# Optimization experiments

Hardware: AMD Instinct MI355X
Metric: run time of the kernel (lower is better)

Reference implementation:

```python
import jax, jax.numpy as jnp
import numpy as np

B, NQ, NK = 4, 2048, 2048
D_MODEL, H, DK, DV, M = 512, 8, 64, 64, 40


def setup_inputs() -> dict:
    key = jax.random.key(0)
    ks = jax.random.split(key, 12)
    s = 0.02  # param init scale (stand-in for xavier)
    return {
        "queries": jax.random.normal(ks[0], (B, NQ, D_MODEL), jnp.float32),
        "keys": jax.random.normal(ks[1], (B, NK, D_MODEL), jnp.float32),
        "values": jax.random.normal(ks[2], (B, NK, D_MODEL), jnp.float32),
        "attention_weights": jax.random.uniform(ks[3], (B, H, NQ, NK), jnp.float32),
        "attention_mask": jax.random.randint(ks[4], (B, H, NQ, NK), 0, 2) == 1,
        "Wq": jax.random.normal(ks[5], (D_MODEL, H * DK), jnp.float32) * s,
        "bq": jnp.zeros((H * DK,), jnp.float32),
        "Wk": jax.random.normal(ks[6], (D_MODEL, H * DK), jnp.float32) * s,
        "bk": jnp.zeros((H * DK,), jnp.float32),
        "Wv": jax.random.normal(ks[7], (D_MODEL, H * DV), jnp.float32) * s,
        "bv": jnp.zeros((H * DV,), jnp.float32),
        "Wo": jax.random.normal(ks[8], (H * DV, D_MODEL), jnp.float32) * s,
        "bo": jnp.zeros((D_MODEL,), jnp.float32),
        "m_k": jax.random.normal(ks[9], (1, M, H * DK), jnp.float32) * s,
        "m_v": jax.random.normal(ks[10], (1, M, H * DV), jnp.float32) * s,
    }


def reference(queries, keys, values, attention_weights, attention_mask,
              Wq, bq, Wk, bk, Wv, bv, Wo, bo, m_k, m_v):
    b, nq, _ = queries.shape
    nk = keys.shape[1]
    # learned memory slots, scaled and broadcast over batch
    mk = jnp.sqrt(jnp.float32(DK)) * jnp.broadcast_to(m_k, (b, M, H * DK))
    mv = jnp.sqrt(jnp.float32(M)) * jnp.broadcast_to(m_v, (b, M, H * DV))
    q = (queries @ Wq + bq).reshape(b, nq, H, DK).transpose(0, 2, 1, 3)      # (b,h,nq,dk)
    k = jnp.concatenate([keys @ Wk + bk, mk], axis=1)
    k = k.reshape(b, nk + M, H, DK).transpose(0, 2, 3, 1)                     # (b,h,dk,nk+m)
    v = jnp.concatenate([values @ Wv + bv, mv], axis=1)
    v = v.reshape(b, nk + M, H, DV).transpose(0, 2, 1, 3)                     # (b,h,nk+m,dv)
    att = jnp.matmul(q, k) / jnp.sqrt(jnp.float32(DK))                        # (b,h,nq,nk+m)
    att_x = att[..., :nk] * attention_weights
    att_x = jnp.where(attention_mask, -jnp.inf, att_x)
    att = jnp.concatenate([att_x, att[..., nk:]], axis=-1)
    att = jax.nn.softmax(att, axis=-1)
    out = jnp.matmul(att, v).transpose(0, 2, 1, 3).reshape(b, nq, H * DV)
    return out @ Wo + bo
```

## Files before the change

kernel.cpp:

```cpp
#include <hip/hip_runtime.h>
#include <hip/hip_bf16.h>
#include <cstdint>
#include <cstddef>

typedef __bf16 bf16_t;
typedef __bf16 bf16x8 __attribute__((ext_vector_type(8)));
typedef __bf16 bf16x4 __attribute__((ext_vector_type(4)));
typedef float  f32x4  __attribute__((ext_vector_type(4)));

#define B_    4
#define NQ_   2048
#define NK_   2048
#define H_    8
#define MSL_  40
#define NKP_  2112
#define SCL2  0.18033688011112042f

#define GLOAD_LDS16(GP, LP)                                                        \
    __builtin_amdgcn_global_load_lds(                                              \
        (const __attribute__((address_space(1))) unsigned int*)(GP),               \
        (__attribute__((address_space(3))) unsigned int*)(LP), 16, 0, 0)

__global__ void detect_mask(const unsigned int* __restrict__ m, int* __restrict__ flag)
{
    __shared__ int found;
    if (threadIdx.x == 0) found = 0;
    __syncthreads();
    unsigned int acc = 0;
    for (int i = threadIdx.x; i < 65536; i += 256)
        acc |= (m[i] & 0xFFFFFF00u);
    if (acc) found = 1;
    __syncthreads();
    if (threadIdx.x == 0) *flag = found;
}

__global__ void transpose_convert4(const float* __restrict__ s0, const float* __restrict__ s1,
                                   const float* __restrict__ s2, const float* __restrict__ s3,
                                   bf16_t* __restrict__ d0, bf16_t* __restrict__ d1,
                                   bf16_t* __restrict__ d2, bf16_t* __restrict__ d3)
{
    const float* src; bf16_t* dst;
    switch (blockIdx.z) {
        case 0:  src = s0; dst = d0; break;
        case 1:  src = s1; dst = d1; break;
        case 2:  src = s2; dst = d2; break;
        default: src = s3; dst = d3; break;
    }
    __shared__ float t[32][33];
    int x  = blockIdx.x * 32 + threadIdx.x;
    int y0 = blockIdx.y * 32 + threadIdx.y;
#pragma unroll
    for (int i = 0; i < 32; i += 8)
        t[threadIdx.y + i][threadIdx.x] = src[(size_t)(y0 + i) * 512 + x];
    __syncthreads();
    int ox  = blockIdx.y * 32 + threadIdx.x;
    int oy0 = blockIdx.x * 32 + threadIdx.y;
#pragma unroll
    for (int i = 0; i < 32; i += 8)
        dst[(size_t)(oy0 + i) * 512 + ox] = (bf16_t)t[threadIdx.x][threadIdx.y + i];
}

__global__ void memfill(const float* __restrict__ m_k, const float* __restrict__ m_v,
                        bf16_t* __restrict__ Kbf, bf16_t* __restrict__ Vt)
{
    int tid = blockIdx.x * 256 + threadIdx.x;
    if (tid < 4 * 64 * 512) {
        int c  = tid & 511;
        int mi = (tid >> 9) & 63;
        int b  = tid >> 15;
        float v = (mi < MSL_) ? 8.0f * m_k[mi * 512 + c] : 0.0f;
        Kbf[((size_t)b * NKP_ + NK_ + mi) * 512 + c] = (bf16_t)v;
    } else {
        int t  = tid - 4 * 64 * 512;
        int mi = t & 63;
        int dv = (t >> 6) & 63;
        int h  = (t >> 12) & 7;
        int b  = t >> 15;
        float v = (mi < MSL_) ? 6.324555320336759f * m_v[mi * 512 + h * 64 + dv] : 0.0f;
        Vt[(((size_t)b * H_ + h) * 64 + dv) * NKP_ + NK_ + mi] = (bf16_t)v;
    }
}

template<int EPI, bool AF32>
__global__ __launch_bounds__(256) void gemm_bt(
    const void* __restrict__ Av, const bf16_t* __restrict__ BT,
    const float* __restrict__ bias, void* __restrict__ dstv, int dstBS)
{
    __shared__ bf16_t As[128][72];
    __shared__ bf16_t Bs[128][72];

    const int tid = threadIdx.x;
    const int w = tid >> 6, l = tid & 63, lg = l >> 4, lr = l & 15;
    const int wr = w >> 1, wc = w & 1;
    const int blockM = blockIdx.x * 128, blockN = blockIdx.y * 128;

    f32x4 acc[4][4];
    const f32x4 zv = {0.f, 0.f, 0.f, 0.f};
#pragma unroll
    for (int i = 0; i < 4; i++)
#pragma unroll
        for (int j = 0; j < 4; j++) acc[i][j] = zv;

    const int ar = tid >> 1;
    const int ac = (tid & 1) * 32;

    for (int k0 = 0; k0 < 512; k0 += 64) {
        if (k0) __syncthreads();
        if constexpr (AF32) {
            const float* arow = (const float*)Av + (size_t)(blockM + ar) * 512 + k0 + ac;
#pragma unroll
            for (int i = 0; i < 8; i++) {
                float4 v = ((const float4*)arow)[i];
                bf16x4 pk = {(bf16_t)v.x, (bf16_t)v.y, (bf16_t)v.z, (bf16_t)v.w};
                *(bf16x4*)&As[ar][ac + i * 4] = pk;
            }
        } else {
            const bf16_t* arow = (const bf16_t*)Av + (size_t)(blockM + ar) * 512 + k0 + ac;
#pragma unroll
            for (int i = 0; i < 4; i++)
                *(uint4*)&As[ar][ac + i * 8] = ((const uint4*)arow)[i];
        }
        {
            const bf16_t* brow = BT + (size_t)(blockN + ar) * 512 + k0 + ac;
#pragma unroll
            for (int i = 0; i < 4; i++)
                *(uint4*)&Bs[ar][ac + i * 8] = ((const uint4*)brow)[i];
        }
        __syncthreads();
#pragma unroll
        for (int ks = 0; ks < 2; ks++) {
            bf16x8 af[4], bfr[4];
#pragma unroll
            for (int mi = 0; mi < 4; mi++)
                af[mi] = *(const bf16x8*)&As[wr * 64 + mi * 16 + lr][ks * 32 + lg * 8];
#pragma unroll
            for (int ni = 0; ni < 4; ni++)
                bfr[ni] = *(const bf16x8*)&Bs[wc * 64 + ni * 16 + lr][ks * 32 + lg * 8];
#pragma unroll
            for (int mi = 0; mi < 4; mi++)
#pragma unroll
                for (int ni = 0; ni < 4; ni++)
                    acc[mi][ni] = __builtin_amdgcn_mfma_f32_16x16x32_bf16(af[mi], bfr[ni], acc[mi][ni], 0, 0, 0);
        }
    }

    const int colbase = blockN + wc * 64;
    float bias_v[4];
#pragma unroll
    for (int ni = 0; ni < 4; ni++) bias_v[ni] = bias[colbase + ni * 16 + lr];

#pragma unroll
    for (int mi = 0; mi < 4; mi++) {
        const int r0 = blockM + wr * 64 + mi * 16 + lg * 4;
#pragma unroll
        for (int ni = 0; ni < 4; ni++) {
            const int c = colbase + ni * 16 + lr;
            f32x4 v = acc[mi][ni];
            if constexpr (EPI == 2) {
                float* dst = (float*)dstv;
#pragma unroll
                for (int j = 0; j < 4; j++)
                    dst[(size_t)(r0 + j) * 512 + c] = v[j] + bias_v[ni];
            } else if constexpr (EPI == 0) {
                bf16_t* dst = (bf16_t*)dstv;
#pragma unroll
                for (int j = 0; j < 4; j++) {
                    int rr = r0 + j;
                    int bb = rr >> 11, nn = rr & 2047;
                    dst[((size_t)bb * dstBS + nn) * 512 + c] = (bf16_t)(v[j] + bias_v[ni]);
                }
            } else {
                bf16_t* dst = (bf16_t*)dstv;
                int bb = r0 >> 11, n0 = r0 & 2047;
                int hh = c >> 6, dv = c & 63;
                bf16x4 pk;
#pragma unroll
                for (int j = 0; j < 4; j++) pk[j] = (bf16_t)(v[j] + bias_v[ni]);
                *(bf16x4*)(dst + (((size_t)bb * H_ + hh) * 64 + dv) * NKP_ + n0) = pk;
            }
        }
    }
}

template<bool BYTEM>
__global__ __launch_bounds__(256) void attn_fused(
    const bf16_t* __restrict__ Qbf, const bf16_t* __restrict__ Kbf,
    const bf16_t* __restrict__ Vt, const float* __restrict__ attw,
    const void* __restrict__ maskv, const int* __restrict__ mflag,
    bf16_t* __restrict__ Obuf)
{
    if ((*mflag != 0) != BYTEM) return;

    __shared__ bf16_t Ks[2][64][64];
    __shared__ bf16_t Vs[2][64][64];
    __shared__ bf16_t Pl[4][1024];

    const int tid = threadIdx.x;
    const int wv = tid >> 6, l = tid & 63, lg = l >> 4, lr = l & 15;
    const int qt = blockIdx.x, h = blockIdx.y, b = blockIdx.z;
    const int q0w = qt * 64 + wv * 16;
    bf16_t* Pw = &Pl[wv][0];

    const size_t bh = (size_t)(b * H_ + h);
    const float* wbase = attw + bh * (size_t)NQ_ * NK_;
    const unsigned char* mb8 = (const unsigned char*)maskv + bh * (size_t)NQ_ * NK_;
    const int* mb32 = (const int*)maskv + bh * (size_t)NQ_ * NK_;
    const char* kbase8 = (const char*)(Kbf + (size_t)b * NKP_ * 512 + h * 64);
    const char* vbase8 = (const char*)(Vt + bh * 64 * (size_t)NKP_);

    bf16x8 qf0 = *(const bf16x8*)&Qbf[((size_t)b * NQ_ + q0w + lr) * 512 + h * 64 + lg * 8];
    bf16x8 qf1 = *(const bf16x8*)&Qbf[((size_t)b * NQ_ + q0w + lr) * 512 + h * 64 + 32 + lg * 8];

    const f32x4 zv = {0.f, 0.f, 0.f, 0.f};
    f32x4 oacc[4];
#pragma unroll
    for (int i = 0; i < 4; i++) oacc[i] = zv;
    float mrun = -INFINITY, lsum = 0.f;
    f32x4 sA[4];

    f32x4 wA[4], wB[4];
    unsigned mA[4], mB[4];
    unsigned miA[16], miB[16];

    const int srow = l >> 3;
    const int scsw = ((l & 7) ^ (srow & 7)) * 16;

#define STAGE(BUF, KCB) do {                                                      \
    _Pragma("unroll") for (int pi_ = 0; pi_ < 2; pi_++) {                         \
        const int p_ = wv * 2 + pi_;                                              \
        const int r_ = p_ * 8 + srow;                                             \
        GLOAD_LDS16(kbase8 + (size_t)((KCB) + r_) * 1024 + scsw,                  \
                    (char*)&Ks[BUF][0][0] + p_ * 1024);                           \
        GLOAD_LDS16(vbase8 + (size_t)r_ * 4224 + (size_t)(KCB) * 2 + scsw,        \
                    (char*)&Vs[BUF][0][0] + p_ * 1024);                           \
    }                                                                             \
} while (0)

#define PREFETCH(KT, WB_, MB_, MIB_) do {                                         \
    const float* wp_ = wbase + (size_t)(q0w + lr) * NK_ + (KT) * 64 + lg * 4;     \
    _Pragma("unroll") for (int n_ = 0; n_ < 4; n_++)                              \
        WB_[n_] = *(const f32x4*)(wp_ + n_ * 16);                                 \
    if constexpr (BYTEM) {                                                        \
        const unsigned char* mp_ = mb8 + (size_t)(q0w + lr) * NK_ + (KT) * 64 + lg * 4; \
        _Pragma("unroll") for (int n_ = 0; n_ < 4; n_++)                          \
            MB_[n_] = *(const unsigned*)(mp_ + n_ * 16);                          \
    } else {                                                                      \
        const int* mp_ = mb32 + (size_t)(q0w + lr) * NK_ + (KT) * 64 + lg * 4;    \
        _Pragma("unroll") for (int n_ = 0; n_ < 4; n_++) {                        \
            uint4 t_ = *(const uint4*)(mp_ + n_ * 16);                            \
            MIB_[n_ * 4 + 0] = t_.x; MIB_[n_ * 4 + 1] = t_.y;                     \
            MIB_[n_ * 4 + 2] = t_.z; MIB_[n_ * 4 + 3] = t_.w; }                   \
    }                                                                             \
} while (0)

#define QKT_LDS(BC) do {                                                          \
    const int sw_ = (lg ^ (lr & 7)) * 8;                                          \
    _Pragma("unroll") for (int n_ = 0; n_ < 4; n_++) {                            \
        const int kr_ = n_ * 16 + lr;                                             \
        f32x4 a_ = zv;                                                            \
        a_ = __builtin_amdgcn_mfma_f32_16x16x32_bf16(*(const bf16x8*)&Ks[BC][kr_][sw_], qf0, a_, 0, 0, 0); \
        a_ = __builtin_amdgcn_mfma_f32_16x16x32_bf16(*(const bf16x8*)&Ks[BC][kr_][sw_ ^ 32], qf1, a_, 0, 0, 0); \
        sA[n_] = a_;                                                              \
    }                                                                             \
} while (0)

#define APPLY(WB_, MB_, MIB_) do {                                                \
    _Pragma("unroll") for (int n_ = 0; n_ < 4; n_++)                              \
    _Pragma("unroll") for (int j_ = 0; j_ < 4; j_++) {                            \
        bool mk_;                                                                 \
        if constexpr (BYTEM) mk_ = ((MB_[n_] >> (8 * j_)) & 0xffu) != 0;          \
        else                 mk_ = (MIB_[n_ * 4 + j_] != 0);                      \
        sA[n_][j_] = mk_ ? -1e30f : sA[n_][j_] * SCL2 * WB_[n_][j_];              \
    }                                                                             \
} while (0)

#define SMPV(BC) do {                                                             \
    float tm_ = sA[0][0];                                                         \
    _Pragma("unroll") for (int n_ = 0; n_ < 4; n_++)                              \
    _Pragma("unroll") for (int j_ = 0; j_ < 4; j_++)                              \
        tm_ = fmaxf(tm_, sA[n_][j_]);                                             \
    tm_ = fmaxf(tm_, __shfl_xor(tm_, 16));                                        \
    tm_ = fmaxf(tm_, __shfl_xor(tm_, 32));                                        \
    float mnew_ = fmaxf(mrun, tm_);                                               \
    float sc_ = exp2f(mrun - mnew_);                                              \
    mrun = mnew_;                                                                 \
    float ts_ = 0.f;                                                              \
    _Pragma("unroll") for (int n_ = 0; n_ < 4; n_++)                              \
    _Pragma("unroll") for (int j_ = 0; j_ < 4; j_++) {                            \
        float p_ = exp2f(sA[n_][j_] - mnew_);                                     \
        sA[n_][j_] = p_; ts_ += p_;                                               \
    }                                                                             \
    ts_ += __shfl_xor(ts_, 16);                                                   \
    ts_ += __shfl_xor(ts_, 32);                                                   \
    lsum = lsum * sc_ + ts_;                                                      \
    _Pragma("unroll") for (int n2_ = 0; n2_ < 4; n2_++) oacc[n2_] *= sc_;         \
    _Pragma("unroll") for (int n_ = 0; n_ < 4; n_++) {                            \
        int c_ = n_ * 2 + (lg >> 1);                                              \
        int qp_ = (lr + 4 * c_) & 15;                                             \
        bf16x4 pk_ = {(bf16_t)sA[n_][0], (bf16_t)sA[n_][1],                       \
                      (bf16_t)sA[n_][2], (bf16_t)sA[n_][3]};                      \
        *(bf16x4*)&Pw[c_ * 128 + qp_ * 8 + (lg & 1) * 4] = pk_;                   \
    }                                                                             \
    bf16x8 pf0_ = *(const bf16x8*)&Pw[lg * 128 + ((lr + 4 * lg) & 15) * 8];       \
    bf16x8 pf1_ = *(const bf16x8*)&Pw[(4 + lg) * 128 + ((lr + 4 * (4 + lg)) & 15) * 8]; \
    const int vsw_ = (lg ^ (lr & 7)) * 8;                                         \
    _Pragma("unroll") for (int n2_ = 0; n2_ < 4; n2_++) {                         \
        const int vr_ = n2_ * 16 + lr;                                            \
        oacc[n2_] = __builtin_amdgcn_mfma_f32_16x16x32_bf16(*(const bf16x8*)&Vs[BC][vr_][vsw_], pf0_, oacc[n2_], 0, 0, 0); \
        oacc[n2_] = __builtin_amdgcn_mfma_f32_16x16x32_bf16(*(const bf16x8*)&Vs[BC][vr_][vsw_ ^ 32], pf1_, oacc[n2_], 0, 0, 0); \
    }                                                                             \
} while (0)

#define BODYT(KT, BC, BN, WB_, MB_, MIB_, WN_, MN_, MIN_) do {                    \
    if ((KT) < 31) STAGE(BN, ((KT) + 1) * 64);                                    \
    QKT_LDS(BC);                                                                  \
    if ((KT) < 31) PREFETCH((KT) + 1, WN_, MN_, MIN_);                            \
    APPLY(WB_, MB_, MIB_);                                                        \
    SMPV(BC);                                                                     \
    __syncthreads();                                                              \
} while (0)

    STAGE(0, 2048);
    PREFETCH(0, wA, mA, miA);
    __syncthreads();

    {
        STAGE(1, 0);
        QKT_LDS(0);
#pragma unroll
        for (int n_ = 0; n_ < 4; n_++)
#pragma unroll
            for (int j_ = 0; j_ < 4; j_++) {
                int kloc = n_ * 16 + lg * 4 + j_;
                sA[n_][j_] = (kloc >= MSL_) ? -1e30f : sA[n_][j_] * SCL2;
            }
        SMPV(0);
        __syncthreads();
    }

    for (int kt = 0; kt < 32; kt += 2) {
        BODYT(kt,     1, 0, wA, mA, miA, wB, mB, miB);
        BODYT(kt + 1, 0, 1, wB, mB, miB, wA, mA, miA);
    }

    float invl = 1.0f / lsum;
#pragma unroll
    for (int n2 = 0; n2 < 4; n2++) {
        bf16x4 ov = {(bf16_t)(oacc[n2][0] * invl), (bf16_t)(oacc[n2][1] * invl),
                     (bf16_t)(oacc[n2][2] * invl), (bf16_t)(oacc[n2][3] * invl)};
        *(bf16x4*)&Obuf[((size_t)b * NQ_ + q0w + lr) * 512 + h * 64 + n2 * 16 + lg * 4] = ov;
    }

#undef STAGE
#undef PREFETCH
#undef QKT_LDS
#undef APPLY
#undef SMPV
#undef BODYT
}

extern "C" void kernel_launch(void* const* d_in, const int* in_sizes, int n_in,
                              void* d_out, int out_size, void* d_ws, size_t ws_size,
                              hipStream_t stream)
{
    const float* queries = (const float*)d_in[0];
    const float* keys    = (const float*)d_in[1];
    const float* values  = (const float*)d_in[2];
    const float* attw    = (const float*)d_in[3];
    const void*  maskv   = d_in[4];
    const float* Wq = (const float*)d_in[5];
    const float* bq = (const float*)d_in[6];
    const float* Wk = (const float*)d_in[7];
    const float* bk = (const float*)d_in[8];
    const float* Wv = (const float*)d_in[9];
    const float* bv = (const float*)d_in[10];
    const float* Wo = (const float*)d_in[11];
    const float* bo = (const float*)d_in[12];
    const float* m_k = (const float*)d_in[13];
    const float* m_v = (const float*)d_in[14];

    char* ws = (char*)d_ws;
    bf16_t* WqT  = (bf16_t*)(ws + 0);
    bf16_t* WkT  = (bf16_t*)(ws + 524288);
    bf16_t* WvT  = (bf16_t*)(ws + 1048576);
    bf16_t* WoT  = (bf16_t*)(ws + 1572864);
    bf16_t* Qbf  = (bf16_t*)(ws + 2097152);
    bf16_t* Kbf  = (bf16_t*)(ws + 10485760);
    bf16_t* Vt   = (bf16_t*)(ws + 19136512);
    bf16_t* Obuf = (bf16_t*)(ws + 27787264);
    int*    mflag = (int*)(ws + 36175872);

    detect_mask<<<1, 256, 0, stream>>>((const unsigned int*)maskv, mflag);
    transpose_convert4<<<dim3(16, 16, 4), dim3(32, 8), 0, stream>>>(
        Wq, Wk, Wv, Wo, WqT, WkT, WvT, WoT);
    memfill<<<1024, 256, 0, stream>>>(m_k, m_v, Kbf, Vt);

    gemm_bt<0, true><<<dim3(64, 4), 256, 0, stream>>>(queries, WqT, bq, Qbf, 2048);
    gemm_bt<0, true><<<dim3(64, 4), 256, 0, stream>>>(keys,    WkT, bk, Kbf, NKP_);
    gemm_bt<1, true><<<dim3(64, 4), 256, 0, stream>>>(values,  WvT, bv, Vt, 0);

    attn_fused<true><<<dim3(32, H_, B_), 256, 0, stream>>>(Qbf, Kbf, Vt, attw, maskv, mflag, Obuf);
    attn_fused<false><<<dim3(32, H_, B_), 256, 0, stream>>>(Qbf, Kbf, Vt, attw, maskv, mflag, Obuf);

    gemm_bt<2, false><<<dim3(64, 4), 256, 0, stream>>>(Obuf, WoT, bo, d_out, 0);
    (void)in_sizes; (void)n_in; (void)out_size; (void)ws_size;
}
```

Baseline: 381.4 us.

## Deepen attention pipeline with two-tile-ahead prefetch and partial vmcnt waits

Restructures the attention main loop so the attention-weight/mask register prefetch runs two tiles ahead instead of one. The end-of-iteration __syncthreads is replaced by a start-of-iteration s_waitcnt vmcnt(8) plus s_barrier, so outstanding global loads are not fully drained. sched_barriers pin the instruction order so the compiler cannot move loads across the staging points. The aim is to hide global memory latency for K/V staging and the attw/mask streams. The hand-tuned vmcnt count is fragile: it depends on exactly how many loads each stage issues, and a wrong count could race on LDS.

```diff
diff --git a/kernel.cpp b/kernel.cpp
--- a/kernel.cpp
+++ b/kernel.cpp
@@ -311,21 +311,30 @@
     }                                                                             \
 } while (0)
 
-#define BODYT(KT, BC, BN, WB_, MB_, MIB_, WN_, MN_, MIN_) do {                    \
-    if ((KT) < 31) STAGE(BN, ((KT) + 1) * 64);                                    \
+#define WAITBAR(WCNT) do {                                                        \
+    asm volatile("s_waitcnt vmcnt(" WCNT ")" ::: "memory");                       \
+    __builtin_amdgcn_s_barrier();                                                 \
+    __builtin_amdgcn_sched_barrier(0);                                            \
+} while (0)
+
+#define BODY(KT, BC, BN, WC_, MC_, MIC_) do {                                     \
+    WAITBAR("8");                                                                 \
+    if ((KT) < 31) { STAGE(BN, ((KT) + 1) * 64); }                                \
+    __builtin_amdgcn_sched_barrier(0);                                            \
     QKT_LDS(BC);                                                                  \
-    if ((KT) < 31) PREFETCH((KT) + 1, WN_, MN_, MIN_);                            \
-    APPLY(WB_, MB_, MIB_);                                                        \
+    APPLY(WC_, MC_, MIC_);                                                        \
+    if ((KT) < 30) { PREFETCH((KT) + 2, WC_, MC_, MIC_); }                        \
     SMPV(BC);                                                                     \
-    __syncthreads();                                                              \
 } while (0)
 
     STAGE(0, 2048);
+    __builtin_amdgcn_sched_barrier(0);
     PREFETCH(0, wA, mA, miA);
-    __syncthreads();
 
     {
+        WAITBAR("8");
         STAGE(1, 0);
+        __builtin_amdgcn_sched_barrier(0);
         QKT_LDS(0);
 #pragma unroll
         for (int n_ = 0; n_ < 4; n_++)
@@ -334,13 +343,20 @@
                 int kloc = n_ * 16 + lg * 4 + j_;
                 sA[n_][j_] = (kloc >= MSL_) ? -1e30f : sA[n_][j_] * SCL2;
             }
+        PREFETCH(1, wB, mB, miB);
         SMPV(0);
-        __syncthreads();
-    }
-
-    for (int kt = 0; kt < 32; kt += 2) {
-        BODYT(kt,     1, 0, wA, mA, miA, wB, mB, miB);
-        BODYT(kt + 1, 0, 1, wB, mB, miB, wA, mA, miA);
+    }
+
+    for (int kt = 0; kt < 30; kt += 2) {
+        BODY(kt,     1, 0, wA, mA, miA);
+        BODY(kt + 1, 0, 1, wB, mB, miB);
+    }
+    BODY(30, 1, 0, wA, mA, miA);
+    {
+        WAITBAR("0");
+        QKT_LDS(0);
+        APPLY(wB, mB, miB);
+        SMPV(0);
     }
 
     float invl = 1.0f / lsum;
@@ -356,7 +372,8 @@
 #undef QKT_LDS
 #undef APPLY
 #undef SMPV
-#undef BODYT
+#undef WAITBAR
+#undef BODY
 }
 
 extern "C" void kernel_launch(void* const* d_in, const int* in_sizes, int n_in,
```

Result: faster. 370.3 us (-2.9%).
